# Kernel optimization log

Hardware: AMD Instinct MI355X
Metric: run time of the kernel (lower is better)

## Reference

```python
import jax, jax.numpy as jnp
import numpy as np


def setup_inputs() -> dict:
    key = jax.random.key(0)
    k1, k2, k3 = jax.random.split(key, 3)
    B, T, J, D = 32, 1024, 128, 256  # D = 2 * input_dim
    ctx_embd = jax.random.normal(k1, (B, T, D), dtype=jnp.float32)
    query_embd = jax.random.normal(k2, (B, J, D), dtype=jnp.float32)
    # nn.Linear(6*input_dim, 1, bias=False) weight flattened: [w1 | w2 | w3], each of size D
    w = jax.random.normal(k3, (3 * D,), dtype=jnp.float32) * (1.0 / np.sqrt(3 * D))
    return {"ctx_embd": ctx_embd, "query_embd": query_embd, "w": w}


def reference(ctx_embd, query_embd, w):
    D = ctx_embd.shape[-1]
    w1, w2, w3 = w[:D], w[D:2 * D], w[2 * D:]
    # Trilinear score S[b,t,j] = ctx.w1 + query.w2 + (ctx*query).w3, decomposed
    # (algebraically identical to Linear(cat(ctx, query, ctx*query))).
    s_ctx = ctx_embd @ w1            # [B, T]
    s_qry = query_embd @ w2          # [B, J]
    s_mul = jnp.einsum('btd,bjd->btj', ctx_embd * w3, query_embd)  # [B, T, J]
    S = s_ctx[:, :, None] + s_qry[:, None, :] + s_mul              # [B, T, J]
    # Context-to-query attention
    a = jax.nn.softmax(S, axis=-1)                                 # [B, T, J]
    c2q = jnp.einsum('btj,bjd->btd', a, query_embd)                # [B, T, D]
    # Query-to-context attention
    b = jax.nn.softmax(jnp.max(S, axis=2), axis=-1)                # [B, T]
    q2c = jnp.einsum('bt,btd->bd', b, ctx_embd)[:, None, :]        # [B, 1, D] broadcast over T
    G = jnp.concatenate(
        [ctx_embd, c2q, ctx_embd * c2q, ctx_embd * q2c], axis=-1)  # [B, T, 4D]
    return G
```

## Files before the change

### kernel.cpp

```cpp
#include <hip/hip_runtime.h>

typedef float f4 __attribute__((ext_vector_type(4)));
typedef short s8v __attribute__((ext_vector_type(8)));

#define B_ 32
#define T_ 1024
#define J_ 128
#define D_ 256

__device__ inline unsigned short f2bf(float x) {
    unsigned int u = __float_as_uint(x);
    u += 0x7fffu + ((u >> 16) & 1u);
    return (unsigned short)(u >> 16);
}

__device__ __forceinline__ void ldsload16(const void* g, void* l) {
    __builtin_amdgcn_global_load_lds(
        (const __attribute__((address_space(1))) void*)g,
        (__attribute__((address_space(3))) void*)l, 16, 0, 0);
}

__global__ __launch_bounds__(256) void k_prep(const float* __restrict__ q, const float* __restrict__ w,
                                              unsigned short* __restrict__ Bqh, float* __restrict__ sq,
                                              float* __restrict__ q2c) {
    int bj = blockIdx.x;
    int d = threadIdx.x;
    if (bj < B_) q2c[bj * D_ + d] = 0.f;
    float qv = q[bj * D_ + d];
    float w1 = w[d], w2 = w[D_ + d], w3 = w[2 * D_ + d];
    Bqh[bj * D_ + d] = f2bf(w3 * qv + w1);
    float p = qv * w2;
#pragma unroll
    for (int m = 32; m >= 1; m >>= 1) p += __shfl_xor(p, m);
    __shared__ float red[4];
    if ((d & 63) == 0) red[d >> 6] = p;
    __syncthreads();
    if (d == 0) sq[bj] = red[0] + red[1] + red[2] + red[3];
}

__global__ __launch_bounds__(256) void k_tq(const float* __restrict__ q,
                                            unsigned short* __restrict__ qTh) {
    __shared__ float t_[64][65];
    int b = blockIdx.x >> 3, jt = (blockIdx.x >> 2) & 1, dt = blockIdx.x & 3;
    const float* qb = q + (b * J_ + jt * 64) * D_ + dt * 64;
#pragma unroll
    for (int i = 0; i < 16; i++) {
        int lin = threadIdx.x + 256 * i;
        int jj = lin >> 6, dd = lin & 63;
        t_[jj][dd] = qb[jj * D_ + dd];
    }
    __syncthreads();
#pragma unroll
    for (int i = 0; i < 16; i++) {
        int lin = threadIdx.x + 256 * i;
        int dd = lin >> 6, jj = lin & 63;
        qTh[(b * D_ + dt * 64 + dd) * J_ + jt * 64 + jj] = f2bf(t_[jj][dd]);
    }
}

__global__ __launch_bounds__(256, 3) void k_main(const float* __restrict__ ctx,
                                                 const unsigned short* __restrict__ Bqh,
                                                 const unsigned short* __restrict__ qTh,
                                                 const float* __restrict__ sq,
                                                 float* __restrict__ M, float* __restrict__ out) {
    __shared__ __align__(16) char lds[41472];
    char* B0 = lds;
    char* B1 = lds + 16384;
    char* Ps = lds + 32768;
    float* sc = (float*)(lds + 40960);

    int b  = blockIdx.x >> 5;
    int t0 = (blockIdx.x & 31) << 5;
    int tid = threadIdx.x;
    int w = tid >> 6, l = tid & 63, lr = l & 15, lq = l >> 4;
    int rg = w & 1, ch = w >> 1;
    int R0 = rg << 4;

    const unsigned short* BqB  = Bqh + b * J_ * D_;
    const unsigned short* qThB = qTh + b * D_ * J_;

    auto stageBq = [&](char* buf, int qt) {
#pragma unroll
        for (int i = 0; i < 4; i++) {
            int g = tid + (i << 8);
            int jr = g >> 3, c = g & 7;
            ldsload16(BqB + jr * D_ + (qt << 6) + ((c ^ (jr & 7)) << 3),
                      buf + (i << 12) + (w << 10));
        }
    };
    auto stageQ = [&](char* buf, int st) {
#pragma unroll
        for (int i = 0; i < 4; i++) {
            int g = tid + (i << 8);
            int dr = g >> 4, c = g & 15;
            ldsload16(qThB + ((st << 6) + dr) * J_ + ((c ^ (dr & 7)) << 3),
                      buf + (i << 12) + (w << 10));
        }
    };

    f4 acc[4];
#pragma unroll
    for (int nf = 0; nf < 4; nf++) acc[nf] = (f4){0.f, 0.f, 0.f, 0.f};

    stageBq(B0, 0);
    stageBq(B1, 1);

    const float* ctxA = ctx + (b * T_ + t0 + R0 + lr) * D_;
    s8v af[8];
    {
        f4 c0[8], c1[8];
#pragma unroll
        for (int k = 0; k < 8; k++) {
            c0[k] = *(const f4*)(ctxA + k * 32 + lq * 8);
            c1[k] = *(const f4*)(ctxA + k * 32 + lq * 8 + 4);
        }
#pragma unroll
        for (int k = 0; k < 8; k++) {
            union { unsigned short u[8]; s8v v; } t;
#pragma unroll
            for (int e = 0; e < 4; e++) { t.u[e] = f2bf(c0[k][e]); t.u[e + 4] = f2bf(c1[k][e]); }
            af[k] = t.v;
        }
    }

    auto mfmaA = [&](char* buf, int qt) {
#pragma unroll
        for (int kk = 0; kk < 2; kk++)
#pragma unroll
            for (int nf = 0; nf < 4; nf++) {
                int jr = (ch << 6) + (nf << 4) + lr;
                s8v bv = *(const s8v*)(buf + (jr << 7) + ((((kk << 2) | lq) ^ (jr & 7)) << 4));
                acc[nf] = __builtin_amdgcn_mfma_f32_16x16x32_bf16(af[(qt << 1) | kk], bv, acc[nf], 0, 0, 0);
            }
    };

    __syncthreads();
    mfmaA(B0, 0);
    __syncthreads();
    stageBq(B0, 2);
    mfmaA(B1, 1);
    __syncthreads();
    stageBq(B1, 3);
    mfmaA(B0, 2);
    __syncthreads();
    stageQ(B0, 0);
    mfmaA(B1, 3);

    float sqv[4];
#pragma unroll
    for (int nf = 0; nf < 4; nf++) sqv[nf] = sq[b * J_ + (ch << 6) + (nf << 4) + lr];
    float mp[4];
#pragma unroll
    for (int r = 0; r < 4; r++) {
        float m = -1e30f;
#pragma unroll
        for (int nf = 0; nf < 4; nf++) { acc[nf][r] += sqv[nf]; m = fmaxf(m, acc[nf][r]); }
#pragma unroll
        for (int msk = 8; msk >= 1; msk >>= 1) m = fmaxf(m, __shfl_xor(m, msk));
        float s = 0.f;
#pragma unroll
        for (int nf = 0; nf < 4; nf++) { float e = __expf(acc[nf][r] - m); acc[nf][r] = e; s += e; }
#pragma unroll
        for (int msk = 8; msk >= 1; msk >>= 1) s += __shfl_xor(s, msk);
        mp[r] = m;
        if (lr == 0) {
            int row = R0 + (lq << 2) + r;
            sc[(row << 2) + (ch << 1)] = m;
            sc[(row << 2) + (ch << 1) + 1] = s;
        }
    }
    __syncthreads();
    stageQ(B1, 1);

#pragma unroll
    for (int r = 0; r < 4; r++) {
        int row = R0 + (lq << 2) + r;
        float m0 = sc[(row << 2)],     s0 = sc[(row << 2) + 1];
        float m1 = sc[(row << 2) + 2], s1 = sc[(row << 2) + 3];
        float m = fmaxf(m0, m1);
        float sum = s0 * __expf(m0 - m) + s1 * __expf(m1 - m);
        float scale = __expf(mp[r] - m) / sum;
#pragma unroll
        for (int nf = 0; nf < 4; nf++) {
            int cc = (ch << 6) + (nf << 4) + lr;
            int chunk = cc >> 3;
            *(unsigned short*)(Ps + row * 256 + ((chunk ^ (row & 7)) << 4) + ((lr & 7) << 1)) =
                f2bf(acc[nf][r] * scale);
        }
        if (ch == 0 && lr == 0) M[b * T_ + t0 + row] = m;
    }
    __syncthreads();

    int dh2 = w >> 1;
    int prow = R0 + lr;
    s8v pf[4];
#pragma unroll
    for (int jk = 0; jk < 4; jk++)
        pf[jk] = *(const s8v*)(Ps + prow * 256 + ((((jk << 2) + lq) ^ (prow & 7)) << 4));

    f4 acc2[8];
#pragma unroll
    for (int ai = 0; ai < 8; ai++) acc2[ai] = (f4){0.f, 0.f, 0.f, 0.f};

    auto mfmaB = [&](char* rb, int s) {
#pragma unroll
        for (int df2 = 0; df2 < 2; df2++) {
            int dr = (dh2 << 5) + (df2 << 4) + lr;
            int ai = (s << 1) + df2;
#pragma unroll
            for (int jk = 0; jk < 4; jk++) {
                s8v bv = *(const s8v*)(rb + (dr << 8) + ((((jk << 2) + lq) ^ (dr & 7)) << 4));
                acc2[ai] = __builtin_amdgcn_mfma_f32_16x16x32_bf16(pf[jk], bv, acc2[ai], 0, 0, 0);
            }
        }
    };

    mfmaB(B0, 0);
    __syncthreads();
    stageQ(B0, 2);
    mfmaB(B1, 1);
    __syncthreads();
    stageQ(B1, 3);
    mfmaB(B0, 2);
    __syncthreads();
    mfmaB(B1, 3);
    __syncthreads();

    float* cq = (float*)lds;
#pragma unroll
    for (int s2 = 0; s2 < 4; s2++)
#pragma unroll
        for (int df2 = 0; df2 < 2; df2++) {
            int col = (s2 << 6) + (dh2 << 5) + (df2 << 4) + lr;
            int ai = (s2 << 1) + df2;
            int chunk = col >> 2;
#pragma unroll
            for (int r = 0; r < 4; r++) {
                int row = R0 + (lq << 2) + r;
                *(float*)((char*)cq + (row << 10) + ((chunk ^ (row & 7)) << 4) + ((col & 3) << 2)) = acc2[ai][r];
            }
        }
    __syncthreads();

    int row = tid >> 3;
    int o = b * T_ + t0 + row;
    const float* crow = ctx + o * D_;
    float* orow = out + o * 1024;
#pragma unroll
    for (int i = 0; i < 8; i++) {
        int col4 = (i << 5) + ((tid & 7) << 2);
        int chunk = col4 >> 2;
        f4 val = *(const f4*)((char*)cq + (row << 10) + ((chunk ^ (row & 7)) << 4));
        f4 cx = *(const f4*)(crow + col4);
        f4 v3 = cx * val;
        __builtin_nontemporal_store(cx, (f4*)(orow + col4));
        __builtin_nontemporal_store(val, (f4*)(orow + 256 + col4));
        __builtin_nontemporal_store(v3, (f4*)(orow + 512 + col4));
    }
}

__global__ __launch_bounds__(256) void k_q2c(const float* __restrict__ ctx, const float* __restrict__ M,
                                             float* __restrict__ q2c) {
    int b = blockIdx.x >> 5, tc = blockIdx.x & 31;
    int tid = threadIdx.x;
    const float* Mb = M + b * T_;

    float v0 = Mb[tid], v1 = Mb[tid + 256], v2 = Mb[tid + 512], v3 = Mb[tid + 768];
    float mx = fmaxf(fmaxf(v0, v1), fmaxf(v2, v3));
#pragma unroll
    for (int m = 32; m >= 1; m >>= 1) mx = fmaxf(mx, __shfl_xor(mx, m));
    __shared__ float rA[4], rB[4], wt[32];
    if ((tid & 63) == 0) rA[tid >> 6] = mx;
    __syncthreads();
    mx = fmaxf(fmaxf(rA[0], rA[1]), fmaxf(rA[2], rA[3]));

    float sm = __expf(v0 - mx) + __expf(v1 - mx) + __expf(v2 - mx) + __expf(v3 - mx);
#pragma unroll
    for (int m = 32; m >= 1; m >>= 1) sm += __shfl_xor(sm, m);
    if ((tid & 63) == 0) rB[tid >> 6] = sm;
    if (tid < 32) wt[tid] = __expf(Mb[tc * 32 + tid] - mx);
    __syncthreads();
    sm = rB[0] + rB[1] + rB[2] + rB[3];

    float acc = 0.f;
    const float* cb = ctx + (b * T_ + tc * 32) * D_ + tid;
#pragma unroll 8
    for (int tt = 0; tt < 32; tt++) acc += wt[tt] * cb[tt * D_];
    atomicAdd(&q2c[b * D_ + tid], acc / sm);
}

__global__ __launch_bounds__(256) void k_out4(const float* __restrict__ ctx, const float* __restrict__ q2c,
                                              float* __restrict__ out) {
    int idx = blockIdx.x * 256 + threadIdx.x;
    int e = idx * 4;
    int b = e >> 18;
    int t = (e >> 8) & 1023;
    int d = e & 255;
    f4 cv = *(const f4*)&ctx[e];
    f4 qv = *(const f4*)&q2c[b * D_ + d];
    f4 r = cv * qv;
    __builtin_nontemporal_store(r, (f4*)&out[(b * T_ + t) * 1024 + 768 + d]);
}

extern "C" void kernel_launch(void* const* d_in, const int* in_sizes, int n_in,
                              void* d_out, int out_size, void* d_ws, size_t ws_size,
                              hipStream_t stream) {
    const float* ctx   = (const float*)d_in[0];
    const float* query = (const float*)d_in[1];
    const float* w     = (const float*)d_in[2];
    float* out = (float*)d_out;

    unsigned short* Bqh = (unsigned short*)d_ws;
    unsigned short* qTh = Bqh + B_ * J_ * D_;
    float* fws = (float*)(qTh + B_ * J_ * D_);
    float* sq  = fws;
    float* M   = fws + 4096;
    float* q2c = fws + 4096 + 32768;

    k_prep<<<B_ * J_, 256, 0, stream>>>(query, w, Bqh, sq, q2c);
    k_tq<<<B_ * 2 * 4, 256, 0, stream>>>(query, qTh);
    k_main<<<B_ * (T_ / 32), 256, 0, stream>>>(ctx, Bqh, qTh, sq, M, out);
    k_q2c<<<B_ * 32, 256, 0, stream>>>(ctx, M, q2c);
    k_out4<<<(B_ * T_ * D_ / 4) / 256, 256, 0, stream>>>(ctx, q2c, out);
}
```

Measured before the change: 67.29 us.

## Fuse query prep kernels and compute q2c partials inside main kernel

Merges the two query preprocessing kernels (bf16 weighted query, score bias, transposed bf16 query) into one kernel that reads the query once with vectorized loads. The main kernel now computes per-block partial softmax-weighted ctx sums and block max/sum, reusing ctx rows while they are likely still cached. A single tail kernel combines the partials and writes the q2c output quarter. This removes the separate q2c and out kernels, the atomics and the q2c zeroing, cutting launch count and ctx re-reads at the cost of extra work per tail block and extra tail work in the main kernel.

```diff
diff --git a/kernel.cpp b/kernel.cpp
--- a/kernel.cpp
+++ b/kernel.cpp
@@ -2,6 +2,8 @@
 
 typedef float f4 __attribute__((ext_vector_type(4)));
 typedef short s8v __attribute__((ext_vector_type(8)));
+typedef unsigned int u2v __attribute__((ext_vector_type(2)));
+typedef unsigned int u4v __attribute__((ext_vector_type(4)));
 
 #define B_ 32
 #define T_ 1024
@@ -20,41 +22,55 @@
         (__attribute__((address_space(3))) void*)l, 16, 0, 0);
 }
 
-__global__ __launch_bounds__(256) void k_prep(const float* __restrict__ q, const float* __restrict__ w,
-                                              unsigned short* __restrict__ Bqh, float* __restrict__ sq,
-                                              float* __restrict__ q2c) {
-    int bj = blockIdx.x;
-    int d = threadIdx.x;
-    if (bj < B_) q2c[bj * D_ + d] = 0.f;
-    float qv = q[bj * D_ + d];
-    float w1 = w[d], w2 = w[D_ + d], w3 = w[2 * D_ + d];
-    Bqh[bj * D_ + d] = f2bf(w3 * qv + w1);
-    float p = qv * w2;
-#pragma unroll
-    for (int m = 32; m >= 1; m >>= 1) p += __shfl_xor(p, m);
-    __shared__ float red[4];
-    if ((d & 63) == 0) red[d >> 6] = p;
-    __syncthreads();
-    if (d == 0) sq[bj] = red[0] + red[1] + red[2] + red[3];
-}
-
-__global__ __launch_bounds__(256) void k_tq(const float* __restrict__ q,
-                                            unsigned short* __restrict__ qTh) {
-    __shared__ float t_[64][65];
-    int b = blockIdx.x >> 3, jt = (blockIdx.x >> 2) & 1, dt = blockIdx.x & 3;
-    const float* qb = q + (b * J_ + jt * 64) * D_ + dt * 64;
-#pragma unroll
-    for (int i = 0; i < 16; i++) {
-        int lin = threadIdx.x + 256 * i;
-        int jj = lin >> 6, dd = lin & 63;
-        t_[jj][dd] = qb[jj * D_ + dd];
-    }
-    __syncthreads();
-#pragma unroll
-    for (int i = 0; i < 16; i++) {
-        int lin = threadIdx.x + 256 * i;
-        int dd = lin >> 6, jj = lin & 63;
-        qTh[(b * D_ + dt * 64 + dd) * J_ + jt * 64 + jj] = f2bf(t_[jj][dd]);
+__global__ __launch_bounds__(256) void k_pre(const float* __restrict__ q, const float* __restrict__ w,
+                                             unsigned short* __restrict__ Bqh, float* __restrict__ sq,
+                                             unsigned short* __restrict__ qTh) {
+    __shared__ float t_[16][260];
+    int b = blockIdx.x >> 3, jt = blockIdx.x & 7;
+    int tid = threadIdx.x;
+    const float* qb = q + (b * J_ + jt * 16) * D_;
+
+#pragma unroll
+    for (int k = 0; k < 4; k++) {
+        int idx = tid + (k << 8);
+        int jj = idx >> 6, d4 = idx & 63;
+        f4 v = *(const f4*)(qb + jj * D_ + (d4 << 2));
+        *(f4*)&t_[jj][d4 << 2] = v;
+        f4 w1v = *(const f4*)(w + (d4 << 2));
+        f4 w3v = *(const f4*)(w + 2 * D_ + (d4 << 2));
+        u2v p;
+        p[0] = (unsigned int)f2bf(w3v[0] * v[0] + w1v[0]) | ((unsigned int)f2bf(w3v[1] * v[1] + w1v[1]) << 16);
+        p[1] = (unsigned int)f2bf(w3v[2] * v[2] + w1v[2]) | ((unsigned int)f2bf(w3v[3] * v[3] + w1v[3]) << 16);
+        *(u2v*)(Bqh + (b * J_ + jt * 16 + jj) * D_ + (d4 << 2)) = p;
+    }
+    __syncthreads();
+
+    {
+        int jj = tid >> 4, dg = tid & 15;
+        float p = 0.f;
+#pragma unroll
+        for (int i = 0; i < 16; i++) {
+            int d = (dg << 4) + i;
+            p += t_[jj][d] * w[D_ + d];
+        }
+#pragma unroll
+        for (int m = 8; m >= 1; m >>= 1) p += __shfl_xor(p, m);
+        if (dg == 0) sq[b * J_ + jt * 16 + jj] = p;
+    }
+
+    {
+        int dd = tid;
+        unsigned int pk[8];
+#pragma unroll
+        for (int i = 0; i < 8; i++) {
+            pk[i] = (unsigned int)f2bf(t_[2 * i][dd]) | ((unsigned int)f2bf(t_[2 * i + 1][dd]) << 16);
+        }
+        u4v v0, v1;
+        v0[0] = pk[0]; v0[1] = pk[1]; v0[2] = pk[2]; v0[3] = pk[3];
+        v1[0] = pk[4]; v1[1] = pk[5]; v1[2] = pk[6]; v1[3] = pk[7];
+        unsigned short* dst = qTh + (b * D_ + dd) * J_ + jt * 16;
+        *(u4v*)dst = v0;
+        *(u4v*)(dst + 8) = v1;
     }
 }
 
@@ -62,12 +78,14 @@
                                                  const unsigned short* __restrict__ Bqh,
                                                  const unsigned short* __restrict__ qTh,
                                                  const float* __restrict__ sq,
-                                                 float* __restrict__ M, float* __restrict__ out) {
-    __shared__ __align__(16) char lds[41472];
+                                                 float* __restrict__ pq2c, float* __restrict__ pms,
+                                                 float* __restrict__ out) {
+    __shared__ __align__(16) char lds[41600];
     char* B0 = lds;
     char* B1 = lds + 16384;
     char* Ps = lds + 32768;
     float* sc = (float*)(lds + 40960);
+    float* mrow = (float*)(lds + 41472);
 
     int b  = blockIdx.x >> 5;
     int t0 = (blockIdx.x & 31) << 5;
@@ -187,7 +205,7 @@
             *(unsigned short*)(Ps + row * 256 + ((chunk ^ (row & 7)) << 4) + ((lr & 7) << 1)) =
                 f2bf(acc[nf][r] * scale);
         }
-        if (ch == 0 && lr == 0) M[b * T_ + t0 + row] = m;
+        if (ch == 0 && lr == 0) mrow[row] = m;
     }
     __syncthreads();
 
@@ -242,64 +260,75 @@
         }
     __syncthreads();
 
+    {
+        int row = tid >> 3;
+        int o = b * T_ + t0 + row;
+        const float* crow = ctx + o * D_;
+        float* orow = out + o * 1024;
+#pragma unroll
+        for (int i = 0; i < 8; i++) {
+            int col4 = (i << 5) + ((tid & 7) << 2);
+            int chunk = col4 >> 2;
+            f4 val = *(const f4*)((char*)cq + (row << 10) + ((chunk ^ (row & 7)) << 4));
+            f4 cx = *(const f4*)(crow + col4);
+            f4 v3 = cx * val;
+            __builtin_nontemporal_store(cx, (f4*)(orow + col4));
+            __builtin_nontemporal_store(val, (f4*)(orow + 256 + col4));
+            __builtin_nontemporal_store(v3, (f4*)(orow + 512 + col4));
+        }
+    }
+
+    {
+        float mblk = -1e30f;
+#pragma unroll 8
+        for (int t = 0; t < 32; t++) mblk = fmaxf(mblk, mrow[t]);
+        float sblk = 0.f, q2a = 0.f;
+        const float* cpart = ctx + (b * T_ + t0) * D_ + tid;
+#pragma unroll 4
+        for (int t = 0; t < 32; t++) {
+            float e = __expf(mrow[t] - mblk);
+            sblk += e;
+            q2a += e * cpart[t * D_];
+        }
+        pq2c[blockIdx.x * 256 + tid] = q2a;
+        if (tid == 0) { pms[blockIdx.x * 2] = mblk; pms[blockIdx.x * 2 + 1] = sblk; }
+    }
+}
+
+__global__ __launch_bounds__(256) void k_tail(const float* __restrict__ ctx,
+                                              const float* __restrict__ pq2c, const float* __restrict__ pms,
+                                              float* __restrict__ out) {
+    int b = blockIdx.x >> 5, tc = blockIdx.x & 31;
+    int tid = threadIdx.x;
+    const float* pm = pms + b * 64;
+
+    float mx = -1e30f;
+#pragma unroll 8
+    for (int i = 0; i < 32; i++) mx = fmaxf(mx, pm[2 * i]);
+    float sm = 0.f, q2 = 0.f;
+#pragma unroll 4
+    for (int i = 0; i < 32; i++) {
+        float e = __expf(pm[2 * i] - mx);
+        sm += pm[2 * i + 1] * e;
+        q2 += e * pq2c[((b << 5) + i) * 256 + tid];
+    }
+    q2 /= sm;
+    __shared__ float q2s[256];
+    q2s[tid] = q2;
+    __syncthreads();
+
     int row = tid >> 3;
-    int o = b * T_ + t0 + row;
+    int o = b * T_ + tc * 32 + row;
     const float* crow = ctx + o * D_;
     float* orow = out + o * 1024;
 #pragma unroll
     for (int i = 0; i < 8; i++) {
         int col4 = (i << 5) + ((tid & 7) << 2);
-        int chunk = col4 >> 2;
-        f4 val = *(const f4*)((char*)cq + (row << 10) + ((chunk ^ (row & 7)) << 4));
         f4 cx = *(const f4*)(crow + col4);
-        f4 v3 = cx * val;
-        __builtin_nontemporal_store(cx, (f4*)(orow + col4));
-        __builtin_nontemporal_store(val, (f4*)(orow + 256 + col4));
-        __builtin_nontemporal_store(v3, (f4*)(orow + 512 + col4));
-    }
-}
-
-__global__ __launch_bounds__(256) void k_q2c(const float* __restrict__ ctx, const float* __restrict__ M,
-                                             float* __restrict__ q2c) {
-    int b = blockIdx.x >> 5, tc = blockIdx.x & 31;
-    int tid = threadIdx.x;
-    const float* Mb = M + b * T_;
-
-    float v0 = Mb[tid], v1 = Mb[tid + 256], v2 = Mb[tid + 512], v3 = Mb[tid + 768];
-    float mx = fmaxf(fmaxf(v0, v1), fmaxf(v2, v3));
-#pragma unroll
-    for (int m = 32; m >= 1; m >>= 1) mx = fmaxf(mx, __shfl_xor(mx, m));
-    __shared__ float rA[4], rB[4], wt[32];
-    if ((tid & 63) == 0) rA[tid >> 6] = mx;
-    __syncthreads();
-    mx = fmaxf(fmaxf(rA[0], rA[1]), fmaxf(rA[2], rA[3]));
-
-    float sm = __expf(v0 - mx) + __expf(v1 - mx) + __expf(v2 - mx) + __expf(v3 - mx);
-#pragma unroll
-    for (int m = 32; m >= 1; m >>= 1) sm += __shfl_xor(sm, m);
-    if ((tid & 63) == 0) rB[tid >> 6] = sm;
-    if (tid < 32) wt[tid] = __expf(Mb[tc * 32 + tid] - mx);
-    __syncthreads();
-    sm = rB[0] + rB[1] + rB[2] + rB[3];
-
-    float acc = 0.f;
-    const float* cb = ctx + (b * T_ + tc * 32) * D_ + tid;
-#pragma unroll 8
-    for (int tt = 0; tt < 32; tt++) acc += wt[tt] * cb[tt * D_];
-    atomicAdd(&q2c[b * D_ + tid], acc / sm);
-}
-
-__global__ __launch_bounds__(256) void k_out4(const float* __restrict__ ctx, const float* __restrict__ q2c,
-                                              float* __restrict__ out) {
-    int idx = blockIdx.x * 256 + threadIdx.x;
-    int e = idx * 4;
-    int b = e >> 18;
-    int t = (e >> 8) & 1023;
-    int d = e & 255;
-    f4 cv = *(const f4*)&ctx[e];
-    f4 qv = *(const f4*)&q2c[b * D_ + d];
-    f4 r = cv * qv;
-    __builtin_nontemporal_store(r, (f4*)&out[(b * T_ + t) * 1024 + 768 + d]);
+        f4 qv = *(const f4*)&q2s[col4];
+        f4 r = cx * qv;
+        __builtin_nontemporal_store(r, (f4*)(orow + 768 + col4));
+    }
 }
 
 extern "C" void kernel_launch(void* const* d_in, const int* in_sizes, int n_in,
@@ -313,13 +342,11 @@
     unsigned short* Bqh = (unsigned short*)d_ws;
     unsigned short* qTh = Bqh + B_ * J_ * D_;
     float* fws = (float*)(qTh + B_ * J_ * D_);
-    float* sq  = fws;
-    float* M   = fws + 4096;
-    float* q2c = fws + 4096 + 32768;
-
-    k_prep<<<B_ * J_, 256, 0, stream>>>(query, w, Bqh, sq, q2c);
-    k_tq<<<B_ * 2 * 4, 256, 0, stream>>>(query, qTh);
-    k_main<<<B_ * (T_ / 32), 256, 0, stream>>>(ctx, Bqh, qTh, sq, M, out);
-    k_q2c<<<B_ * 32, 256, 0, stream>>>(ctx, M, q2c);
-    k_out4<<<(B_ * T_ * D_ / 4) / 256, 256, 0, stream>>>(ctx, q2c, out);
-}
+    float* sq   = fws;
+    float* pq2c = fws + 4096;
+    float* pms  = fws + 4096 + 1024 * 256;
+
+    k_pre<<<B_ * 8, 256, 0, stream>>>(query, w, Bqh, sq, qTh);
+    k_main<<<B_ * (T_ / 32), 256, 0, stream>>>(ctx, Bqh, qTh, sq, pq2c, pms, out);
+    k_tail<<<B_ * 32, 256, 0, stream>>>(ctx, pq2c, pms, out);
+}
```

After: 70.17 us. 1.04x slower.
